# Kernel optimization log

Measured on AMD Instinct MI355X. Metric: run time of the kernel, lower is better.

The kernel has to match this reference:

```python
import jax, jax.numpy as jnp
import numpy as np

COST_CLASS = 1.0
COST_POINT = 1.0


def _linear_sum_assignment(cost):
    """Pure-numpy Jonker-Volgenant / Hungarian (e-maxx formulation).
    Emulates scipy.optimize.linear_sum_assignment for a dense float cost matrix.
    Returns (row_ind, col_ind) with row_ind sorted ascending.
    """
    cost = np.asarray(cost, dtype=np.float64)
    transposed = cost.shape[0] > cost.shape[1]
    if transposed:
        cost = cost.T
    n, m = cost.shape  # n <= m
    INF = np.inf
    u = np.zeros(n + 1)
    v = np.zeros(m + 1)
    p = np.zeros(m + 1, dtype=np.int64)  # p[j] = row (1-indexed) matched to col j
    for i in range(1, n + 1):
        p[0] = i
        j0 = 0
        minv = np.full(m + 1, INF)
        way = np.zeros(m + 1, dtype=np.int64)
        used = np.zeros(m + 1, dtype=bool)
        while True:
            used[j0] = True
            i0 = p[j0]
            cur = cost[i0 - 1, :] - u[i0] - v[1:]
            free = ~used[1:]
            upd = free & (cur < minv[1:])
            minv[1:][upd] = cur[upd]
            way[1:][upd] = j0
            masked = np.where(free, minv[1:], INF)
            j1 = int(np.argmin(masked)) + 1
            delta = masked[j1 - 1]
            u[p[used]] += delta
            v[used] -= delta
            minv[1:][free] -= delta
            j0 = j1
            if p[j0] == 0:
                break
        while j0 != 0:
            j1 = way[j0]
            p[j0] = p[j1]
            j0 = j1
    ans = np.zeros(n, dtype=np.int64)  # ans[row] = col
    for j in range(1, m + 1):
        if p[j] > 0:
            ans[p[j] - 1] = j - 1
    if transposed:
        # rows of the original matrix are ans values; sort by original row index
        order = np.argsort(ans)
        return ans[order], np.arange(n, dtype=np.int64)[order]
    return np.arange(n, dtype=np.int64), ans


def _cost_matrix(pred_logits, pred_points, tgt_labels, tgt_points):
    bs, Q, C = pred_logits.shape
    T = tgt_labels.shape[1]
    out_prob = jax.nn.softmax(pred_logits.reshape(bs * Q, C), axis=-1)   # [bs*Q, C]
    out_points = pred_points.reshape(bs * Q, -1)                          # [bs*Q, 2]
    tgt_ids = tgt_labels.reshape(-1)                                      # [bs*T]
    tgt_pts = tgt_points.reshape(bs * T, -1).astype(jnp.float32)          # [bs*T, 2]
    cost_class = -out_prob[:, tgt_ids]                                    # [bs*Q, bs*T]
    # L1 cdist
    cost_point = jnp.sum(jnp.abs(out_points[:, None, :] - tgt_pts[None, :, :]), axis=-1)
    Cfull = COST_POINT * cost_point + COST_CLASS * cost_class             # [bs*Q, bs*T]
    # per-batch diagonal blocks (what the scipy split selects): [bs, Q, T]
    C4 = Cfull.reshape(bs, Q, bs, T)
    Cb = C4[jnp.arange(bs), :, jnp.arange(bs), :]
    return Cb


def setup_inputs() -> dict:
    key = jax.random.key(0)
    k1, k2, k3, k4 = jax.random.split(key, 4)
    bs, Q, C, T = 16, 1024, 92, 128
    return {
        "pred_logits": jax.random.normal(k1, (bs, Q, C), dtype=jnp.float32),
        "pred_points": jax.random.uniform(k2, (bs, Q, 2), dtype=jnp.float32),
        "tgt_labels": jax.random.randint(k3, (bs, T), 0, C, dtype=jnp.int64),
        "tgt_points": jax.random.uniform(k4, (bs, T, 2), dtype=jnp.float32),
    }


def reference(pred_logits, pred_points, tgt_labels, tgt_points):
    Cb = _cost_matrix(pred_logits, pred_points, tgt_labels, tgt_points)   # [bs, Q, T]
    Cnp = np.asarray(jax.device_get(Cb))
    rows, cols = [], []
    for b in range(Cnp.shape[0]):  # structural loop over batch for the assignment
        r, c = _linear_sum_assignment(Cnp[b])
        rows.append(r)
        cols.append(c)
    row_idx = jnp.asarray(np.stack(rows))  # [bs, T] selected query indices (sorted)
    col_idx = jnp.asarray(np.stack(cols))  # [bs, T] matched target indices
    return Cb, row_idx, col_idx
```

## Files before the change

### kernel.cpp

```cpp
#include <hip/hip_runtime.h>
#include <hip/hip_bf16.h>
#include <math.h>

#define BS 16
#define Q 1024
#define CC 92
#define T 128
#define M 1024
#define NR 128
#define NQB 16

__global__ __launch_bounds__(256) void prep_kernel(
    const float* __restrict__ logits,
    const float* __restrict__ ppts,
    const int*   __restrict__ tlab,
    const float* __restrict__ tpts,
    float* __restrict__ Cb,
    float* __restrict__ CbT,
    unsigned long long* __restrict__ part)
{
    const int blk = blockIdx.x;
    const int b   = blk & 15;
    const int qb  = blk >> 4;
    const int q0  = qb * 64;
    const int tid = threadIdx.x;
    const int lane = tid & 63;

    __shared__ float lg[64 * CC];
    __shared__ float tile[128][68];
    __shared__ float tx_sh[T], ty_sh[T];
    __shared__ int   lab_sh[T];
    __shared__ float mx_sh[64], inv_sh[64], px_sh[64], py_sh[64];

    if (tid < T) {
        lab_sh[tid] = tlab[b * T + tid];
        tx_sh[tid]  = tpts[(b * T + tid) * 2 + 0];
        ty_sh[tid]  = tpts[(b * T + tid) * 2 + 1];
    }
    if (tid < 64) {
        px_sh[tid] = ppts[((size_t)b * Q + q0 + tid) * 2 + 0];
        py_sh[tid] = ppts[((size_t)b * Q + q0 + tid) * 2 + 1];
    }
    const float* lbase = logits + ((size_t)b * Q + q0) * CC;
    for (int idx = tid; idx < 64 * CC; idx += 256) lg[idx] = lbase[idx];
    __syncthreads();

    {
        const int w = tid >> 6;
        for (int s = 0; s < 16; ++s) {
            const int ql = w * 16 + s;
            const float* c = &lg[ql * CC];
            float l0 = c[lane];
            float l1 = (lane + 64 < CC) ? c[lane + 64] : -INFINITY;
            float mx = fmaxf(l0, l1);
            #pragma unroll
            for (int off = 32; off > 0; off >>= 1)
                mx = fmaxf(mx, __shfl_down(mx, off));
            mx = __shfl(mx, 0);
            float es = expf(l0 - mx) + ((lane + 64 < CC) ? expf(l1 - mx) : 0.0f);
            #pragma unroll
            for (int off = 32; off > 0; off >>= 1) es += __shfl_down(es, off);
            es = __shfl(es, 0);
            if (lane == 0) { mx_sh[ql] = mx; inv_sh[ql] = 1.0f / es; }
        }
    }
    __syncthreads();

    {
        const int ql = tid >> 2;
        const int tc = tid & 3;
        const float px = px_sh[ql], py = py_sh[ql];
        const float mx = mx_sh[ql], inv = inv_sh[ql];
        const float* lgq = &lg[ql * CC];
        float* cbrow = Cb + ((size_t)b * Q + q0 + ql) * T + tc * 32;
        #pragma unroll
        for (int k = 0; k < 8; ++k) {
            float4 o;
            #pragma unroll
            for (int e = 0; e < 4; ++e) {
                const int t = tc * 32 + 4 * k + e;
                const int labv = lab_sh[t];
                float prob = expf(lgq[labv] - mx) * inv;
                float cp   = fabsf(px - tx_sh[t]) + fabsf(py - ty_sh[t]);
                float val  = cp - prob;
                (&o.x)[e] = val;
                tile[t][ql] = val;
            }
            ((float4*)cbrow)[k] = o;
        }
    }
    __syncthreads();

    {
        const int rg = tid >> 4;
        const int c4 = tid & 15;
        #pragma unroll
        for (int it = 0; it < 8; ++it) {
            const int t = it * 16 + rg;
            float4 v = *(const float4*)&tile[t][4 * c4];
            *(float4*)(CbT + ((size_t)b * NR + t) * Q + q0 + 4 * c4) = v;

            unsigned long long bk = ~0ull;
            const float* vf = (const float*)&v;
            #pragma unroll
            for (int e = 0; e < 4; ++e) {
                unsigned bits = __float_as_uint(vf[e]);
                unsigned mono = (bits & 0x80000000u) ? ~bits
                                                     : (bits | 0x80000000u);
                const int j = q0 + 4 * c4 + e;
                unsigned long long key =
                    ((unsigned long long)mono << 10) | (unsigned)j;
                bk = (key < bk) ? key : bk;
            }
            #pragma unroll
            for (int off = 1; off < 16; off <<= 1) {
                unsigned long long ok = __shfl_xor(bk, off);
                bk = (ok < bk) ? ok : bk;
            }
            if (c4 == 0) part[((size_t)b * NQB + qb) * NR + t] = bk;
        }
    }
}

__global__ __launch_bounds__(256) void cost_kernel(
    const float* __restrict__ logits, const float* __restrict__ ppts,
    const int* __restrict__ tlab, const float* __restrict__ tpts,
    float* __restrict__ Cb)
{
    const int blk  = blockIdx.x;
    const int b    = blk >> 8;
    const int wave = threadIdx.x >> 6;
    const int lane = threadIdx.x & 63;
    const int q    = (blk & 255) * 4 + wave;

    __shared__ float tx_sh[T], ty_sh[T];
    __shared__ int   lab_sh[T];
    __shared__ float logit_sh[4][CC];

    if (threadIdx.x < T) {
        lab_sh[threadIdx.x] = tlab[b * T + threadIdx.x];
        tx_sh[threadIdx.x]  = tpts[(b * T + threadIdx.x) * 2 + 0];
        ty_sh[threadIdx.x]  = tpts[(b * T + threadIdx.x) * 2 + 1];
    }
    const float* lrow = logits + ((size_t)b * Q + q) * CC;
    float l0 = lrow[lane];
    float l1 = (lane + 64 < CC) ? lrow[lane + 64] : -INFINITY;
    logit_sh[wave][lane] = l0;
    if (lane + 64 < CC) logit_sh[wave][lane + 64] = l1;

    float mx = fmaxf(l0, l1);
    #pragma unroll
    for (int off = 32; off > 0; off >>= 1) mx = fmaxf(mx, __shfl_down(mx, off));
    mx = __shfl(mx, 0);
    float es = expf(l0 - mx) + ((lane + 64 < CC) ? expf(l1 - mx) : 0.0f);
    #pragma unroll
    for (int off = 32; off > 0; off >>= 1) es += __shfl_down(es, off);
    es = __shfl(es, 0);
    const float inv = 1.0f / es;
    const float px = ppts[((size_t)b * Q + q) * 2 + 0];
    const float py = ppts[((size_t)b * Q + q) * 2 + 1];
    __syncthreads();
    float* outrow = Cb + ((size_t)b * Q + q) * T;
    #pragma unroll
    for (int t = lane; t < T; t += 64) {
        int   labv = lab_sh[t];
        float prob = expf(logit_sh[wave][labv] - mx) * inv;
        float cp   = fabsf(px - tx_sh[t]) + fabsf(py - ty_sh[t]);
        outrow[t]  = cp - prob;
    }
}

#define DPP_UMIN_STEP(x, ctrl)                                              \
    {                                                                       \
        unsigned _t = (unsigned)__builtin_amdgcn_update_dpp(                \
            (int)(x), (int)(x), (ctrl), 0xF, 0xF, false);                   \
        (x) = ((x) < _t) ? (x) : _t;                                        \
    }

#define DPP_UMIN_REDUCE(x)                                                  \
    DPP_UMIN_STEP(x, 0x111); DPP_UMIN_STEP(x, 0x112);                       \
    DPP_UMIN_STEP(x, 0x114); DPP_UMIN_STEP(x, 0x118);                       \
    DPP_UMIN_STEP(x, 0x142); DPP_UMIN_STEP(x, 0x143);

#define DPP_UMIN2_STEP(x1, x2, ctrl)                                        \
    {                                                                       \
        unsigned _t1 = (unsigned)__builtin_amdgcn_update_dpp(               \
            (int)(x1), (int)(x1), (ctrl), 0xF, 0xF, false);                 \
        unsigned _t2 = (unsigned)__builtin_amdgcn_update_dpp(               \
            (int)(x2), (int)(x2), (ctrl), 0xF, 0xF, false);                 \
        unsigned _hi = ((x1) > _t1) ? (x1) : _t1;                           \
        unsigned _lo2 = ((x2) < _t2) ? (x2) : _t2;                          \
        (x1) = ((x1) < _t1) ? (x1) : _t1;                                   \
        (x2) = (_hi < _lo2) ? _hi : _lo2;                                   \
    }

#define DPP_UMIN2_REDUCE(x1, x2)                                            \
    DPP_UMIN2_STEP(x1, x2, 0x111); DPP_UMIN2_STEP(x1, x2, 0x112);           \
    DPP_UMIN2_STEP(x1, x2, 0x114); DPP_UMIN2_STEP(x1, x2, 0x118);           \
    DPP_UMIN2_STEP(x1, x2, 0x142); DPP_UMIN2_STEP(x1, x2, 0x143);

__device__ __forceinline__ unsigned mono_enc(float f) {
    unsigned b = __float_as_uint(f);
    return (b & 0x80000000u) ? ~b : (b | 0x80000000u);
}
__device__ __forceinline__ float mono_dec(unsigned m) {
    unsigned b = (m & 0x80000000u) ? (m ^ 0x80000000u) : ~m;
    return __uint_as_float(b);
}

template<int USET>
__global__ __launch_bounds__(64) void solve_kernel(
    const float* __restrict__ Cb,
    const float* __restrict__ CbT,
    const unsigned long long* __restrict__ part,
    float* __restrict__ out_rows,
    float* __restrict__ out_cols)
{
    const int b    = blockIdx.x;
    const int lane = threadIdx.x;

    __shared__ int    row4col[M];
    __shared__ int    col4row[NR];
    __shared__ float  u_sh[NR];
    __shared__ int    path_lds[M];
    __shared__ int    SRr[NR];
    __shared__ float  SRd[NR];
    __shared__ int    minj_sh[NR];
    __shared__ int    claim[M];

    const float* CbB  = Cb  + (size_t)b * Q * T;
    const float* CbTB = CbT + (size_t)b * NR * Q;

    for (int j = lane; j < M;  j += 64) { row4col[j] = -1; claim[j] = 0x7fffffff; }
    for (int i = lane; i < NR; i += 64) col4row[i] = -1;

    if (part) {
        #pragma unroll
        for (int r2 = 0; r2 < 2; ++r2) {
            const int r = lane + 64 * r2;
            const unsigned long long* pr = part + (size_t)b * NQB * NR + r;
            unsigned long long k = pr[0];
            #pragma unroll
            for (int i = 1; i < NQB; ++i) {
                unsigned long long o = pr[(size_t)i * NR];
                k = (o < k) ? o : k;
            }
            minj_sh[r] = (int)(k & 1023u);
            u_sh[r] = mono_dec((unsigned)(k >> 10));
        }
    } else {
        for (int i = lane; i < NR; i += 64) { minj_sh[i] = -1; u_sh[i] = 0.0f; }
    }
    __syncthreads();

    if (part) {
        #pragma unroll
        for (int r2 = 0; r2 < 2; ++r2) {
            const int r = lane + 64 * r2;
            atomicMin(&claim[minj_sh[r]], r);
        }
        __syncthreads();
        #pragma unroll
        for (int r2 = 0; r2 < 2; ++r2) {
            const int r = lane + 64 * r2;
            const int mj = minj_sh[r];
            if (claim[mj] == r) { col4row[r] = mj; row4col[mj] = r; }
        }
        __syncthreads();
    }

    const float FINF = INFINITY;
    float v_[16], dist_[16];
    #pragma unroll
    for (int k = 0; k < 16; ++k) v_[k] = 0.0f;

    {
        unsigned long long am0 = ~__ballot(col4row[lane] >= 0);
        unsigned long long am1 = ~__ballot(col4row[lane + 64] >= 0);
        for (int half = 0; half < 2; ++half) {
            unsigned long long mask = half ? am1 : am0;
            while (mask) {
                int cur = __ffsll(mask) - 1 + 64 * half;
                mask &= mask - 1;

                for (int step = 0; step < 48; ++step) {
                    const float ucur = u_sh[cur];

                    float4 c4[4];
                    if (USET) {
                        const float4* row =
                            (const float4*)(CbTB + (size_t)cur * Q);
                        #pragma unroll
                        for (int g = 0; g < 4; ++g) c4[g] = row[lane + 64 * g];
                    } else {
                        const float* col = CbB + cur;
                        #pragma unroll
                        for (int g = 0; g < 4; ++g) {
                            float* cf = (float*)&c4[g];
                            #pragma unroll
                            for (int e = 0; e < 4; ++e)
                                cf[e] = col[(size_t)(256*g + 4*lane + e) * T];
                        }
                    }

                    float m1l = FINF, m2l = FINF; int j1l = 0;
                    #pragma unroll
                    for (int g = 0; g < 4; ++g) {
                        const float* cf = (const float*)&c4[g];
                        #pragma unroll
                        for (int e = 0; e < 4; ++e) {
                            const int k = 4 * g + e;
                            const int j = 256 * g + 4 * lane + e;
                            float r = cf[e] - ucur - v_[k];
                            if (r < m1l) { m2l = m1l; m1l = r; j1l = j; }
                            else if (r < m2l) { m2l = r; }
                        }
                    }

                    const int cand = row4col[j1l];

                    const unsigned lm1 = mono_enc(m1l);
                    unsigned e1 = lm1;
                    unsigned e2 = mono_enc(m2l);
                    DPP_UMIN2_REDUCE(e1, e2);
                    const unsigned g1 =
                        (unsigned)__builtin_amdgcn_readlane((int)e1, 63);
                    const unsigned g2 =
                        (unsigned)__builtin_amdgcn_readlane((int)e2, 63);
                    const float m1 = mono_dec(g1);
                    const float m2 = mono_dec(g2);

                    const unsigned long long bm = __ballot(lm1 == g1);
                    const int winner = __ffsll(bm) - 1;
                    const int j1   = __builtin_amdgcn_readlane(j1l, winner);
                    const int disp = __builtin_amdgcn_readlane(cand, winner);

                    if (lane == 0) u_sh[cur] = ucur + m2;
                    if (((j1 >> 2) & 63) == lane) {
                        const int k = ((j1 >> 8) << 2) | (j1 & 3);
                        v_[k] -= (m2 - m1);
                    }

                    if (lane == 0) {
                        row4col[j1]  = cur;
                        col4row[cur] = j1;
                        if (disp >= 0) col4row[disp] = -1;
                    }
                    if (disp < 0) { cur = -1; break; }
                    cur = disp;
                }
            }
        }
    }

    unsigned long long um0 = ~__ballot(col4row[lane] >= 0);
    unsigned long long um1 = ~__ballot(col4row[lane + 64] >= 0);

    for (int half = 0; half < 2; ++half) {
        unsigned long long mask = half ? um1 : um0;
        while (mask) {
            const int curRow = __ffsll(mask) - 1 + 64 * half;
            mask &= mask - 1;

            #pragma unroll
            for (int k = 0; k < 16; ++k) dist_[k] = FINF;
            unsigned used  = 0;
            float    minVal = 0.0f;
            int      i_s  = curRow;
            int      sink = -1;
            int      cnt  = 0;

            for (int guard = 0; guard <= M; ++guard) {
                const float ui = u_sh[i_s];
                const float s  = minVal - ui;

                float4 c4[4];
                if (USET) {
                    const float4* row = (const float4*)(CbTB + (size_t)i_s * Q);
                    #pragma unroll
                    for (int g = 0; g < 4; ++g) c4[g] = row[lane + 64 * g];
                } else {
                    const float* col = CbB + i_s;
                    #pragma unroll
                    for (int g = 0; g < 4; ++g) {
                        float* cf = (float*)&c4[g];
                        #pragma unroll
                        for (int e = 0; e < 4; ++e)
                            cf[e] = col[(size_t)(256 * g + 4 * lane + e) * T];
                    }
                }

                float lmin = FINF; int lidx = 0;
                #pragma unroll
                for (int g = 0; g < 4; ++g) {
                    const float* cf = (const float*)&c4[g];
                    #pragma unroll
                    for (int e = 0; e < 4; ++e) {
                        const int k = 4 * g + e;
                        const int j = 256 * g + 4 * lane + e;
                        const bool fr = ((used >> k) & 1u) == 0u;
                        float r = s + cf[e] - v_[k];
                        if (fr && r < dist_[k]) {
                            dist_[k] = r;
                            path_lds[256 * g + 64 * e + lane] = i_s;
                        }
                        float a = fr ? dist_[k] : FINF;
                        if (a < lmin) { lmin = a; lidx = j; }
                    }
                }

                const int cand = row4col[lidx];

                unsigned lmono = mono_enc(lmin);
                unsigned rmin = lmono;
                DPP_UMIN_REDUCE(rmin);
                const unsigned gmin =
                    (unsigned)__builtin_amdgcn_readlane((int)rmin, 63);

                const unsigned long long bmask = __ballot(lmono == gmin);
                const int winner = __ffsll(bmask) - 1;

                minVal = __uint_as_float(
                    (unsigned)__builtin_amdgcn_readlane(
                        (int)__float_as_uint(lmin), winner));
                const int jstar = __builtin_amdgcn_readlane(lidx, winner);

                if (((jstar >> 2) & 63) == lane)
                    used |= (1u << (((jstar >> 8) << 2) | (jstar & 3)));

                const int ra = __builtin_amdgcn_readlane(cand, winner);
                if (ra == -1) { sink = jstar; break; }
                if (lane == 0 && cnt < NR) { SRr[cnt] = ra; SRd[cnt] = minVal; }
                cnt++;
                i_s = ra;
            }

            #pragma unroll
            for (int k = 0; k < 16; ++k)
                if ((used >> k) & 1u) v_[k] += dist_[k] - minVal;

            if (lane == 0) u_sh[curRow] += minVal;
            for (int t = lane; t < cnt; t += 64)
                u_sh[SRr[t]] += minVal - SRd[t];

            if (lane == 0) {
                int j = sink;
                for (int g2 = 0; g2 < NR + 2; ++g2) {
                    int pi = path_lds[((j >> 8) << 8) | ((j & 3) << 6) |
                                      ((j >> 2) & 63)];
                    row4col[j] = pi;
                    int jn = col4row[pi];
                    col4row[pi] = j;
                    if (pi == curRow) break;
                    j = jn;
                }
            }
            __syncthreads();
        }
    }

    int base = 0;
    #pragma unroll
    for (int g = 0; g < 4; ++g) {
        int tv[4], mt[4];
        #pragma unroll
        for (int e = 0; e < 4; ++e) {
            const int j = 256 * g + 4 * lane + e;
            tv[e] = row4col[j];
            mt[e] = (tv[e] >= 0);
        }
        unsigned long long B[4];
        #pragma unroll
        for (int e = 0; e < 4; ++e) B[e] = __ballot(mt[e] != 0);
        const unsigned long long low = (1ull << lane) - 1ull;
        int below = base;
        #pragma unroll
        for (int e = 0; e < 4; ++e) below += __popcll(B[e] & low);
        int local = 0;
        #pragma unroll
        for (int e = 0; e < 4; ++e) {
            if (mt[e]) {
                const int rank = below + local;
                const int j = 256 * g + 4 * lane + e;
                out_rows[b * NR + rank] = (float)j;
                out_cols[b * NR + rank] = (float)tv[e];
                ++local;
            }
        }
        #pragma unroll
        for (int e = 0; e < 4; ++e) base += __popcll(B[e]);
    }
}

extern "C" void kernel_launch(void* const* d_in, const int* in_sizes, int n_in,
                              void* d_out, int out_size, void* d_ws, size_t ws_size,
                              hipStream_t stream) {
    const float* logits = (const float*)d_in[0];
    const float* ppts   = (const float*)d_in[1];
    const int*   tlab   = (const int*)  d_in[2];
    const float* tpts   = (const float*)d_in[3];

    float* Cb   = (float*)d_out;
    float* rows = Cb + (size_t)BS * Q * T;
    float* cols = rows + (size_t)BS * T;

    float* CbT = (float*)d_ws;
    unsigned long long* part =
        (unsigned long long*)((char*)d_ws + (size_t)BS * NR * Q * sizeof(float));

    const size_t need = (size_t)BS * NR * Q * sizeof(float)
                      + (size_t)BS * NQB * NR * sizeof(unsigned long long);

    if (ws_size >= need) {
        prep_kernel<<<BS * NQB, 256, 0, stream>>>(logits, ppts, tlab, tpts,
                                                  Cb, CbT, part);
        solve_kernel<1><<<BS, 64, 0, stream>>>(Cb, CbT, part, rows, cols);
    } else {
        cost_kernel<<<4096, 256, 0, stream>>>(logits, ppts, tlab, tpts, Cb);
        solve_kernel<0><<<BS, 64, 0, stream>>>(Cb, CbT, nullptr, rows, cols);
    }
}
```

Baseline: 124.7 us.

## Process two auction rows per wavefront using half-wave segments and LDS dual prices

Moves the column dual prices v from per-lane registers into LDS so both half-wavefronts can read them. The initial auction/greedy phase now handles two unassigned rows at once, each 32-lane segment scanning a full 1024-column row, with a segmented DPP reduction and explicit resolution when both rows bid for the same column. The aim is to halve the serial bid iterations in the warm-start phase. In exchange, every iteration now reads v from LDS, each lane does twice the per-lane work, and the bidding order differs, which could change the warm start and the number of later augmentations.

```diff
diff --git a/kernel.cpp b/kernel.cpp
--- a/kernel.cpp
+++ b/kernel.cpp
@@ -194,10 +194,10 @@
         (x2) = (_hi < _lo2) ? _hi : _lo2;                                   \
     }
 
-#define DPP_UMIN2_REDUCE(x1, x2)                                            \
+#define DPP_UMIN2_REDUCE_SEG32(x1, x2)                                      \
     DPP_UMIN2_STEP(x1, x2, 0x111); DPP_UMIN2_STEP(x1, x2, 0x112);           \
     DPP_UMIN2_STEP(x1, x2, 0x114); DPP_UMIN2_STEP(x1, x2, 0x118);           \
-    DPP_UMIN2_STEP(x1, x2, 0x142); DPP_UMIN2_STEP(x1, x2, 0x143);
+    DPP_UMIN2_STEP(x1, x2, 0x142);
 
 __device__ __forceinline__ unsigned mono_enc(float f) {
     unsigned b = __float_as_uint(f);
@@ -222,6 +222,7 @@
     __shared__ int    row4col[M];
     __shared__ int    col4row[NR];
     __shared__ float  u_sh[NR];
+    __shared__ float  v_lds[M];
     __shared__ int    path_lds[M];
     __shared__ int    SRr[NR];
     __shared__ float  SRd[NR];
@@ -231,7 +232,9 @@
     const float* CbB  = Cb  + (size_t)b * Q * T;
     const float* CbTB = CbT + (size_t)b * NR * Q;
 
-    for (int j = lane; j < M;  j += 64) { row4col[j] = -1; claim[j] = 0x7fffffff; }
+    for (int j = lane; j < M;  j += 64) {
+        row4col[j] = -1; claim[j] = 0x7fffffff; v_lds[j] = 0.0f;
+    }
     for (int i = lane; i < NR; i += 64) col4row[i] = -1;
 
     if (part) {
@@ -270,85 +273,131 @@
     }
 
     const float FINF = INFINITY;
-    float v_[16], dist_[16];
-    #pragma unroll
-    for (int k = 0; k < 16; ++k) v_[k] = 0.0f;
 
     {
-        unsigned long long am0 = ~__ballot(col4row[lane] >= 0);
-        unsigned long long am1 = ~__ballot(col4row[lane + 64] >= 0);
-        for (int half = 0; half < 2; ++half) {
-            unsigned long long mask = half ? am1 : am0;
-            while (mask) {
-                int cur = __ffsll(mask) - 1 + 64 * half;
-                mask &= mask - 1;
-
-                for (int step = 0; step < 48; ++step) {
-                    const float ucur = u_sh[cur];
-
-                    float4 c4[4];
-                    if (USET) {
-                        const float4* row =
-                            (const float4*)(CbTB + (size_t)cur * Q);
-                        #pragma unroll
-                        for (int g = 0; g < 4; ++g) c4[g] = row[lane + 64 * g];
-                    } else {
-                        const float* col = CbB + cur;
-                        #pragma unroll
-                        for (int g = 0; g < 4; ++g) {
-                            float* cf = (float*)&c4[g];
-                            #pragma unroll
-                            for (int e = 0; e < 4; ++e)
-                                cf[e] = col[(size_t)(256*g + 4*lane + e) * T];
-                        }
+        unsigned long long pm0 = ~__ballot(col4row[lane] >= 0);
+        unsigned long long pm1 = ~__ballot(col4row[lane + 64] >= 0);
+
+        const int seg = lane >> 5;
+        const int sl  = lane & 31;
+
+        for (int round = 0; round < 192; ++round) {
+            if (!(pm0 | pm1)) break;
+
+            int cur0 = -1, cur1 = -1;
+            if (pm0)      { cur0 = __ffsll(pm0) - 1;      pm0 &= pm0 - 1; }
+            else          { cur0 = __ffsll(pm1) - 1 + 64; pm1 &= pm1 - 1; }
+            if (pm0)      { cur1 = __ffsll(pm0) - 1;      pm0 &= pm0 - 1; }
+            else if (pm1) { cur1 = __ffsll(pm1) - 1 + 64; pm1 &= pm1 - 1; }
+            const bool dual = (cur1 >= 0);
+            const int myrow = (seg && dual) ? cur1 : cur0;
+
+            const float uc = u_sh[myrow];
+
+            float4 c4[8];
+            if (USET) {
+                const float4* rp = (const float4*)(CbTB + (size_t)myrow * Q);
+                #pragma unroll
+                for (int g = 0; g < 8; ++g) c4[g] = rp[32 * g + sl];
+            } else {
+                const float* col = CbB + myrow;
+                #pragma unroll
+                for (int g = 0; g < 8; ++g) {
+                    float* cf = (float*)&c4[g];
+                    #pragma unroll
+                    for (int e = 0; e < 4; ++e)
+                        cf[e] = col[(size_t)(128 * g + 4 * sl + e) * T];
+                }
+            }
+            float4 v4[8];
+            const float4* vp = (const float4*)v_lds;
+            #pragma unroll
+            for (int g = 0; g < 8; ++g) v4[g] = vp[32 * g + sl];
+
+            float m1l = FINF, m2l = FINF; int j1l = 0;
+            #pragma unroll
+            for (int g = 0; g < 8; ++g) {
+                const float* cf = (const float*)&c4[g];
+                const float* vf = (const float*)&v4[g];
+                #pragma unroll
+                for (int e = 0; e < 4; ++e) {
+                    const int j = 128 * g + 4 * sl + e;
+                    float r = cf[e] - uc - vf[e];
+                    if (r < m1l) { m2l = m1l; m1l = r; j1l = j; }
+                    else if (r < m2l) { m2l = r; }
+                }
+            }
+
+            const int cand = row4col[j1l];
+
+            const unsigned lm1 = mono_enc(m1l);
+            unsigned e1 = lm1, e2 = mono_enc(m2l);
+            DPP_UMIN2_REDUCE_SEG32(e1, e2);
+            const unsigned g1_0 = (unsigned)__builtin_amdgcn_readlane((int)e1, 31);
+            const unsigned g2_0 = (unsigned)__builtin_amdgcn_readlane((int)e2, 31);
+            const unsigned g1_1 = (unsigned)__builtin_amdgcn_readlane((int)e1, 63);
+            const unsigned g2_1 = (unsigned)__builtin_amdgcn_readlane((int)e2, 63);
+
+            const unsigned long long b0 =
+                __ballot((seg == 0) && (lm1 == g1_0));
+            const unsigned long long b1 =
+                __ballot((seg == 1) && (lm1 == g1_1));
+            const int w0 = __ffsll(b0) - 1;
+            const int w1 = b1 ? (__ffsll(b1) - 1) : -1;
+
+            const int j1_0   = __builtin_amdgcn_readlane(j1l, w0);
+            const int disp0  = __builtin_amdgcn_readlane(cand, w0);
+            const float m1_0 = mono_dec(g1_0), m2_0 = mono_dec(g2_0);
+            const float d0   = m2_0 - m1_0;
+
+            int j1_1 = -1, disp1 = -1; float m1_1 = 0, m2_1 = 0, d1 = 0;
+            if (dual && w1 >= 0) {
+                j1_1  = __builtin_amdgcn_readlane(j1l, w1);
+                disp1 = __builtin_amdgcn_readlane(cand, w1);
+                m1_1 = mono_dec(g1_1); m2_1 = mono_dec(g2_1);
+                d1 = m2_1 - m1_1;
+            }
+
+            if (lane == 0)  u_sh[cur0] = uc + m2_0;
+            if (dual && lane == 32) u_sh[cur1] = uc + m2_1;
+
+            const bool conflict = dual && (j1_1 == j1_0);
+
+            if (!conflict) {
+                if (lane == 0) {
+                    v_lds[j1_0] -= d0;
+                    row4col[j1_0] = cur0; col4row[cur0] = j1_0;
+                    if (disp0 >= 0) col4row[disp0] = -1;
+                    if (dual) {
+                        v_lds[j1_1] -= d1;
+                        row4col[j1_1] = cur1; col4row[cur1] = j1_1;
+                        if (disp1 >= 0) col4row[disp1] = -1;
                     }
-
-                    float m1l = FINF, m2l = FINF; int j1l = 0;
-                    #pragma unroll
-                    for (int g = 0; g < 4; ++g) {
-                        const float* cf = (const float*)&c4[g];
-                        #pragma unroll
-                        for (int e = 0; e < 4; ++e) {
-                            const int k = 4 * g + e;
-                            const int j = 256 * g + 4 * lane + e;
-                            float r = cf[e] - ucur - v_[k];
-                            if (r < m1l) { m2l = m1l; m1l = r; j1l = j; }
-                            else if (r < m2l) { m2l = r; }
-                        }
-                    }
-
-                    const int cand = row4col[j1l];
-
-                    const unsigned lm1 = mono_enc(m1l);
-                    unsigned e1 = lm1;
-                    unsigned e2 = mono_enc(m2l);
-                    DPP_UMIN2_REDUCE(e1, e2);
-                    const unsigned g1 =
-                        (unsigned)__builtin_amdgcn_readlane((int)e1, 63);
-                    const unsigned g2 =
-                        (unsigned)__builtin_amdgcn_readlane((int)e2, 63);
-                    const float m1 = mono_dec(g1);
-                    const float m2 = mono_dec(g2);
-
-                    const unsigned long long bm = __ballot(lm1 == g1);
-                    const int winner = __ffsll(bm) - 1;
-                    const int j1   = __builtin_amdgcn_readlane(j1l, winner);
-                    const int disp = __builtin_amdgcn_readlane(cand, winner);
-
-                    if (lane == 0) u_sh[cur] = ucur + m2;
-                    if (((j1 >> 2) & 63) == lane) {
-                        const int k = ((j1 >> 8) << 2) | (j1 & 3);
-                        v_[k] -= (m2 - m1);
-                    }
-
-                    if (lane == 0) {
-                        row4col[j1]  = cur;
-                        col4row[cur] = j1;
-                        if (disp >= 0) col4row[disp] = -1;
-                    }
-                    if (disp < 0) { cur = -1; break; }
-                    cur = disp;
-                }
+                }
+                if (disp0 >= 0) {
+                    if (disp0 < 64) pm0 |= (1ull << disp0);
+                    else            pm1 |= (1ull << (disp0 - 64));
+                }
+                if (dual && disp1 >= 0) {
+                    if (disp1 < 64) pm0 |= (1ull << disp1);
+                    else            pm1 |= (1ull << (disp1 - 64));
+                }
+            } else {
+                const bool w_is0 = (d0 >= d1);
+                const int  W  = w_is0 ? cur0 : cur1;
+                const int  L  = w_is0 ? cur1 : cur0;
+                const float dW = w_is0 ? d0 : d1;
+                if (lane == 0) {
+                    v_lds[j1_0] -= dW;
+                    row4col[j1_0] = W; col4row[W] = j1_0;
+                    if (disp0 >= 0) col4row[disp0] = -1;
+                }
+                if (disp0 >= 0) {
+                    if (disp0 < 64) pm0 |= (1ull << disp0);
+                    else            pm1 |= (1ull << (disp0 - 64));
+                }
+                if (L < 64) pm0 |= (1ull << L);
+                else        pm1 |= (1ull << (L - 64));
             }
         }
     }
@@ -356,6 +405,7 @@
     unsigned long long um0 = ~__ballot(col4row[lane] >= 0);
     unsigned long long um1 = ~__ballot(col4row[lane + 64] >= 0);
 
+    float dist_[16];
     for (int half = 0; half < 2; ++half) {
         unsigned long long mask = half ? um1 : um0;
         while (mask) {
@@ -389,17 +439,22 @@
                             cf[e] = col[(size_t)(256 * g + 4 * lane + e) * T];
                     }
                 }
+                float4 v4[4];
+                const float4* vp = (const float4*)v_lds;
+                #pragma unroll
+                for (int g = 0; g < 4; ++g) v4[g] = vp[64 * g + lane];
 
                 float lmin = FINF; int lidx = 0;
                 #pragma unroll
                 for (int g = 0; g < 4; ++g) {
                     const float* cf = (const float*)&c4[g];
+                    const float* vf = (const float*)&v4[g];
                     #pragma unroll
                     for (int e = 0; e < 4; ++e) {
                         const int k = 4 * g + e;
                         const int j = 256 * g + 4 * lane + e;
                         const bool fr = ((used >> k) & 1u) == 0u;
-                        float r = s + cf[e] - v_[k];
+                        float r = s + cf[e] - vf[e];
                         if (fr && r < dist_[k]) {
                             dist_[k] = r;
                             path_lds[256 * g + 64 * e + lane] = i_s;
@@ -436,8 +491,12 @@
             }
 
             #pragma unroll
-            for (int k = 0; k < 16; ++k)
-                if ((used >> k) & 1u) v_[k] += dist_[k] - minVal;
+            for (int k = 0; k < 16; ++k) {
+                if ((used >> k) & 1u) {
+                    const int j = 256 * (k >> 2) + 4 * lane + (k & 3);
+                    v_lds[j] += dist_[k] - minVal;
+                }
+            }
 
             if (lane == 0) u_sh[curRow] += minVal;
             for (int t = lane; t < cnt; t += 64)
```

Result: slower. 129.0 us (+3.5%).

## Add LDS direct-mapped row cache and prefetch next auction row

Applied to the files above, without the earlier changes.

Adds a 12-slot direct-mapped shared-memory cache of cost rows, keyed by row index, that both the auction phase and the shortest-augmenting-path phase use. In the auction loop, the next row (the displaced one) is loaded from global memory and from the cache before the current step's bookkeeping finishes, so its latency overlaps that work. The path and claim arrays are merged into one buffer to make room in LDS. Each row fetch now always issues both a global load and an LDS read and selects between them, so the global latency is not actually skipped on a hit, and extra LDS traffic and register pressure are added.

```diff
diff --git a/kernel.cpp b/kernel.cpp
--- a/kernel.cpp
+++ b/kernel.cpp
@@ -9,6 +9,7 @@
 #define M 1024
 #define NR 128
 #define NQB 16
+#define NSLOT 12
 
 __global__ __launch_bounds__(256) void prep_kernel(
     const float* __restrict__ logits,
@@ -219,20 +220,49 @@
     const int b    = blockIdx.x;
     const int lane = threadIdx.x;
 
+    __shared__ float  rowcache[NSLOT][M];
+    __shared__ int    tag_lds[NSLOT];
     __shared__ int    row4col[M];
+    __shared__ int    aux[M];
     __shared__ int    col4row[NR];
     __shared__ float  u_sh[NR];
-    __shared__ int    path_lds[M];
     __shared__ int    SRr[NR];
     __shared__ float  SRd[NR];
     __shared__ int    minj_sh[NR];
-    __shared__ int    claim[M];
 
     const float* CbB  = Cb  + (size_t)b * Q * T;
     const float* CbTB = CbT + (size_t)b * NR * Q;
 
-    for (int j = lane; j < M;  j += 64) { row4col[j] = -1; claim[j] = 0x7fffffff; }
+    auto gload = [&](float4* dst, int row) {
+        if (USET) {
+            const float4* rp = (const float4*)(CbTB + (size_t)row * Q);
+            #pragma unroll
+            for (int g = 0; g < 4; ++g) dst[g] = rp[lane + 64 * g];
+        } else {
+            const float* col = CbB + row;
+            #pragma unroll
+            for (int g = 0; g < 4; ++g) {
+                float* cf = (float*)&dst[g];
+                #pragma unroll
+                for (int e = 0; e < 4; ++e)
+                    cf[e] = col[(size_t)(256 * g + 4 * lane + e) * T];
+            }
+        }
+    };
+    auto cread = [&](float4* dst, int sl) {
+        const float4* cp = (const float4*)&rowcache[sl][0];
+        #pragma unroll
+        for (int g = 0; g < 4; ++g) dst[g] = cp[lane + 64 * g];
+    };
+    auto cwrite = [&](const float4* src, int sl) {
+        float4* wp = (float4*)&rowcache[sl][0];
+        #pragma unroll
+        for (int g = 0; g < 4; ++g) wp[lane + 64 * g] = src[g];
+    };
+
+    for (int j = lane; j < M;  j += 64) { row4col[j] = -1; aux[j] = 0x7fffffff; }
     for (int i = lane; i < NR; i += 64) col4row[i] = -1;
+    if (lane < NSLOT) tag_lds[lane] = -1;
 
     if (part) {
         #pragma unroll
@@ -257,14 +287,14 @@
         #pragma unroll
         for (int r2 = 0; r2 < 2; ++r2) {
             const int r = lane + 64 * r2;
-            atomicMin(&claim[minj_sh[r]], r);
+            atomicMin(&aux[minj_sh[r]], r);
         }
         __syncthreads();
         #pragma unroll
         for (int r2 = 0; r2 < 2; ++r2) {
             const int r = lane + 64 * r2;
             const int mj = minj_sh[r];
-            if (claim[mj] == r) { col4row[r] = mj; row4col[mj] = r; }
+            if (aux[mj] == r) { col4row[r] = mj; row4col[mj] = r; }
         }
         __syncthreads();
     }
@@ -283,26 +313,25 @@
                 int cur = __ffsll(mask) - 1 + 64 * half;
                 mask &= mask - 1;
 
+                float4 c4[4];
+                float ucur;
+                {
+                    const int sl = cur % NSLOT;
+                    const int tg = tag_lds[sl];
+                    float4 g4[4], l4[4];
+                    gload(g4, cur);
+                    cread(l4, sl);
+                    ucur = u_sh[cur];
+                    const bool hit = (tg == cur);
+                    #pragma unroll
+                    for (int g = 0; g < 4; ++g) c4[g] = hit ? l4[g] : g4[g];
+                    if (!hit) {
+                        cwrite(c4, sl);
+                        if (lane == 0) tag_lds[sl] = cur;
+                    }
+                }
+
                 for (int step = 0; step < 48; ++step) {
-                    const float ucur = u_sh[cur];
-
-                    float4 c4[4];
-                    if (USET) {
-                        const float4* row =
-                            (const float4*)(CbTB + (size_t)cur * Q);
-                        #pragma unroll
-                        for (int g = 0; g < 4; ++g) c4[g] = row[lane + 64 * g];
-                    } else {
-                        const float* col = CbB + cur;
-                        #pragma unroll
-                        for (int g = 0; g < 4; ++g) {
-                            float* cf = (float*)&c4[g];
-                            #pragma unroll
-                            for (int e = 0; e < 4; ++e)
-                                cf[e] = col[(size_t)(256*g + 4*lane + e) * T];
-                        }
-                    }
-
                     float m1l = FINF, m2l = FINF; int j1l = 0;
                     #pragma unroll
                     for (int g = 0; g < 4; ++g) {
@@ -335,19 +364,35 @@
                     const int j1   = __builtin_amdgcn_readlane(j1l, winner);
                     const int disp = __builtin_amdgcn_readlane(cand, winner);
 
+                    const int nxt = (disp >= 0) ? disp : 0;
+                    const int sln = nxt % NSLOT;
+                    const int tgn = tag_lds[sln];
+                    float4 g4[4], l4[4];
+                    gload(g4, nxt);
+                    cread(l4, sln);
+                    const float unext = u_sh[nxt];
+
                     if (lane == 0) u_sh[cur] = ucur + m2;
                     if (((j1 >> 2) & 63) == lane) {
                         const int k = ((j1 >> 8) << 2) | (j1 & 3);
                         v_[k] -= (m2 - m1);
                     }
-
                     if (lane == 0) {
                         row4col[j1]  = cur;
                         col4row[cur] = j1;
                         if (disp >= 0) col4row[disp] = -1;
                     }
-                    if (disp < 0) { cur = -1; break; }
-                    cur = disp;
+                    if (disp < 0) break;
+
+                    cur  = disp;
+                    ucur = unext;
+                    const bool hit = (tgn == nxt);
+                    #pragma unroll
+                    for (int g = 0; g < 4; ++g) c4[g] = hit ? l4[g] : g4[g];
+                    if (!hit) {
+                        cwrite(c4, sln);
+                        if (lane == 0) tag_lds[sln] = cur;
+                    }
                 }
             }
         }
@@ -375,18 +420,18 @@
                 const float s  = minVal - ui;
 
                 float4 c4[4];
-                if (USET) {
-                    const float4* row = (const float4*)(CbTB + (size_t)i_s * Q);
+                {
+                    const int sl = i_s % NSLOT;
+                    const int tg = tag_lds[sl];
+                    float4 g4[4], l4[4];
+                    gload(g4, i_s);
+                    cread(l4, sl);
+                    const bool hit = (tg == i_s);
                     #pragma unroll
-                    for (int g = 0; g < 4; ++g) c4[g] = row[lane + 64 * g];
-                } else {
-                    const float* col = CbB + i_s;
-                    #pragma unroll
-                    for (int g = 0; g < 4; ++g) {
-                        float* cf = (float*)&c4[g];
-                        #pragma unroll
-                        for (int e = 0; e < 4; ++e)
-                            cf[e] = col[(size_t)(256 * g + 4 * lane + e) * T];
+                    for (int g = 0; g < 4; ++g) c4[g] = hit ? l4[g] : g4[g];
+                    if (!hit) {
+                        cwrite(c4, sl);
+                        if (lane == 0) tag_lds[sl] = i_s;
                     }
                 }
 
@@ -402,7 +447,7 @@
                         float r = s + cf[e] - v_[k];
                         if (fr && r < dist_[k]) {
                             dist_[k] = r;
-                            path_lds[256 * g + 64 * e + lane] = i_s;
+                            aux[256 * g + 64 * e + lane] = i_s;
                         }
                         float a = fr ? dist_[k] : FINF;
                         if (a < lmin) { lmin = a; lidx = j; }
@@ -446,8 +491,8 @@
             if (lane == 0) {
                 int j = sink;
                 for (int g2 = 0; g2 < NR + 2; ++g2) {
-                    int pi = path_lds[((j >> 8) << 8) | ((j & 3) << 6) |
-                                      ((j >> 2) & 63)];
+                    int pi = aux[((j >> 8) << 8) | ((j & 3) << 6) |
+                                 ((j >> 2) & 63)];
                     row4col[j] = pi;
                     int jn = col4row[pi];
                     col4row[pi] = j;
```

Result: slower. 132.1 us (+5.9%).
